# Performance work log

Measured on AMD Instinct MI355X. Metric: run time of the kernel, lower is better.

The kernel has to match this reference:

```python
import jax, jax.numpy as jnp
import numpy as np

# Instant-NGP style multi-level hash encoding constants (match init_kwargs)
N_LEVELS = 16
N_ENC = 16384          # per-level hashmap size (power of two)
N_EMBED = 2
MIN_RES = 16
MAX_RES = 512
HIDDEN = 64
P1 = np.uint32(2654435761)  # spatial hash primes (Instant-NGP)
P2 = np.uint32(805459861)


def _resolutions():
    b = np.exp((np.log(MAX_RES) - np.log(MIN_RES)) / (N_LEVELS - 1))
    return [int(np.floor(MIN_RES * b ** l)) for l in range(N_LEVELS)]


def _hash_encode(x, tables):
    """x: (B,3) in [-1,1]; tables: (L, T, E). Returns (B, L*E)."""
    feats = []
    for l, res in enumerate(_resolutions()):
        xg = (x + 1.0) * (0.5 * (res - 1))          # map [-1,1] -> [0, res-1]
        x0f = jnp.floor(xg)
        w = xg - x0f                                # (B,3) trilinear weights
        i0 = jnp.clip(x0f.astype(jnp.int32), 0, res - 1)
        i1 = jnp.clip(i0 + 1, 0, res - 1)
        dense = (res ** 3) <= N_ENC                 # small levels index densely
        feat = jnp.zeros((x.shape[0], N_EMBED), dtype=x.dtype)
        for cz in (0, 1):
            for cy in (0, 1):
                for cx in (0, 1):
                    ix = i1[:, 0] if cx else i0[:, 0]
                    iy = i1[:, 1] if cy else i0[:, 1]
                    iz = i1[:, 2] if cz else i0[:, 2]
                    if dense:
                        idx = ix + res * (iy + res * iz)
                    else:
                        idx = (ix.astype(jnp.uint32)
                               ^ (iy.astype(jnp.uint32) * P1)
                               ^ (iz.astype(jnp.uint32) * P2)) & np.uint32(N_ENC - 1)
                        idx = idx.astype(jnp.int32)
                    wc = ((w[:, 0] if cx else 1.0 - w[:, 0])
                          * (w[:, 1] if cy else 1.0 - w[:, 1])
                          * (w[:, 2] if cz else 1.0 - w[:, 2]))
                    feat = feat + wc[:, None] * tables[l, idx]
        feats.append(feat)
    return jnp.concatenate(feats, axis=-1)          # (B, 32)


def setup_inputs() -> dict:
    key = jax.random.key(0)
    ks = jax.random.split(key, 10)
    B = 1048576
    x = jax.random.uniform(ks[0], (B, 3), minval=-1.0, maxval=1.0)
    tables = jax.random.uniform(ks[1], (N_LEVELS, N_ENC, N_EMBED),
                                minval=-1e-4, maxval=1e-4)

    def lin(k, fin, fout):
        s = 1.0 / np.sqrt(fin)
        kw, kb = jax.random.split(k)
        return (jax.random.uniform(kw, (fin, fout), minval=-s, maxval=s),
                jax.random.uniform(kb, (fout,), minval=-s, maxval=s))

    w1, b1 = lin(ks[2], N_LEVELS * N_EMBED, HIDDEN)
    w2, b2 = lin(ks[3], HIDDEN, HIDDEN)
    w3, b3 = lin(ks[4], HIDDEN, 16)
    cw1, cb1 = lin(ks[5], 16, HIDDEN)
    cw2, cb2 = lin(ks[6], HIDDEN, HIDDEN)
    cw3, cb3 = lin(ks[7], HIDDEN, HIDDEN)
    cw4, cb4 = lin(ks[8], HIDDEN, 3)
    return {"x": x, "tables": tables,
            "w1": w1, "b1": b1, "w2": w2, "b2": b2, "w3": w3, "b3": b3,
            "cw1": cw1, "cb1": cb1, "cw2": cw2, "cb2": cb2,
            "cw3": cw3, "cb3": cb3, "cw4": cw4, "cb4": cb4}


def reference(x, tables, w1, b1, w2, b2, w3, b3,
              cw1, cb1, cw2, cb2, cw3, cb3, cw4, cb4):
    h = _hash_encode(x, tables)                     # (B, 32)
    d = jax.nn.relu(h @ w1 + b1)
    d = jax.nn.relu(d @ w2 + b2)
    d = d @ w3 + b3                                 # (B, 16)
    c = jax.nn.relu(d @ cw1 + cb1)
    c = jax.nn.relu(c @ cw2 + cb2)
    c = jax.nn.relu(c @ cw3 + cb3)
    c = jax.nn.sigmoid(c @ cw4 + cb4)               # is_hdr=False -> sigmoid
    sigma = jnp.exp(d[:, 0])                        # (B,)
    return sigma, c
```

## Files before the change

kernel.cpp:

```cpp
#include <hip/hip_runtime.h>

typedef __bf16 bf8 __attribute__((ext_vector_type(8)));
typedef float f4 __attribute__((ext_vector_type(4)));
typedef float f32x16 __attribute__((ext_vector_type(16)));
typedef unsigned short us4 __attribute__((ext_vector_type(4)));
typedef unsigned int u32x4 __attribute__((ext_vector_type(4)));

#define MFMA16(a,b,c) __builtin_amdgcn_mfma_f32_16x16x32_bf16((a),(b),(c),0,0,0)
#define MFMA32(a,b,c) __builtin_amdgcn_mfma_f32_32x32x16_bf16((a),(b),(c),0,0,0)

#define BLOCK 512
#define NWAVE 8

__device__ __forceinline__ unsigned short f2bfu(float f){
  __bf16 h = (__bf16)f;
  union { __bf16 b; unsigned short u; } v; v.b = h; return v.u;
}
__device__ __forceinline__ float ubfu(unsigned int u16){
  union { unsigned int i; float f; } v; v.i = u16 << 16; return v.f;
}

__device__ __forceinline__ void wfence(){
  asm volatile("s_waitcnt lgkmcnt(0)" ::: "memory");
}

#define SBAR() __builtin_amdgcn_sched_barrier(0)

#define OFF_W1   0
#define OFF_W2   2048
#define OFF_W3   6144
#define OFF_CW1  7168
#define OFF_CW2  8192
#define OFF_CW3  12288
#define OFF_CW4  16384
#define OFF_ACT  17408
#define ACT_STRIDE 72
#define SMEM_US  (17408 + NWAVE*16*ACT_STRIDE)

#define BO_B1  0
#define BO_B2  64
#define BO_B3  128
#define BO_CB1 144
#define BO_CB2 208
#define BO_CB3 272
#define BO_CB4 336

template<int FIN,int FOUT,int KS,int MT>
__device__ __forceinline__ void stage_w(const float* w, unsigned short* dst){
  const int total = KS*MT*512;
  for (int e = threadIdx.x; e < total; e += BLOCK){
    int chunk = e >> 9;
    int s = chunk / MT, t = chunk % MT;
    int le = e & 511;
    int lane = le >> 3, j = le & 7;
    int q = lane >> 4, m = lane & 15;
    int i = s*32 + q*8 + j;
    int o = t*16 + m;
    dst[e] = (i < FIN && o < FOUT) ? f2bfu(w[i*FOUT + o]) : (unsigned short)0;
  }
}

__device__ __forceinline__ void stage_cw1(const float* w, unsigned short* dst){
  for (int e = threadIdx.x; e < 1024; e += BLOCK){
    int t = e >> 8;
    int le = e & 255;
    int lane = le >> 3, j = e & 7;
    int q = lane >> 4, m = lane & 15;
    dst[e] = f2bfu(w[(q*8+j)*64 + t*16 + m]);
  }
}

__device__ __forceinline__ void layer64(const unsigned short* wlds, const unsigned short* bias,
                                        unsigned short* act, int lane, bool relu){
  const int q = lane >> 4, m = lane & 15;
  bf8 b0 = *(const bf8*)(act + m*ACT_STRIDE + q*8);
  bf8 b1 = *(const bf8*)(act + m*ACT_STRIDE + 32 + q*8);
  f4 acc[4];
#pragma unroll
  for (int t = 0; t < 4; ++t){
    f4 c = {0.f,0.f,0.f,0.f};
    c = MFMA16(*(const bf8*)(wlds + ((0*4+t)*64+lane)*8), b0, c);
    c = MFMA16(*(const bf8*)(wlds + ((1*4+t)*64+lane)*8), b1, c);
    acc[t] = c;
  }
#pragma unroll
  for (int t = 0; t < 4; ++t){
    us4 bb = *(const us4*)(bias + t*16 + q*4);
    us4 pk;
#pragma unroll
    for (int r = 0; r < 4; ++r){
      float v = acc[t][r] + ubfu(bb[r]);
      if (relu) v = fmaxf(v, 0.f);
      pk[r] = f2bfu(v);
    }
    *(us4*)(act + m*ACT_STRIDE + t*16 + q*4) = pk;
  }
}

#define STAGE_ALL_WEIGHTS()                                                  \
  stage_w<32,64,1,4>(w1,  smem+OFF_W1);                                      \
  stage_w<64,64,2,4>(w2,  smem+OFF_W2);                                      \
  stage_w<64,16,2,1>(w3,  smem+OFF_W3);                                      \
  stage_cw1(cw1, smem+OFF_CW1);                                              \
  stage_w<64,64,2,4>(cw2, smem+OFF_CW2);                                     \
  stage_w<64,64,2,4>(cw3, smem+OFF_CW3);                                     \
  stage_w<64, 3,2,1>(cw4, smem+OFF_CW4);                                     \
  {                                                                          \
    int t = threadIdx.x;                                                     \
    if (t < 64){                                                             \
      sbias[BO_B1 +t] = f2bfu(b1[t]);                                        \
      sbias[BO_B2 +t] = f2bfu(b2[t]);                                        \
      sbias[BO_CB1+t] = f2bfu(cb1[t]);                                       \
      sbias[BO_CB2+t] = f2bfu(cb2[t]);                                       \
      sbias[BO_CB3+t] = f2bfu(cb3[t]);                                       \
    }                                                                        \
    if (t < 16) sbias[BO_B3+t] = f2bfu(b3[t]);                               \
    if (t < 3)  sbias[BO_CB4+t] = f2bfu(cb4[t]);                             \
  }

#define MLP_BODY(bfrag, gp)                                                  \
    {                                                                        \
      f4 acc[4];                                                             \
      _Pragma("unroll")                                                      \
      for (int t = 0; t < 4; ++t){                                           \
        f4 c = {0.f,0.f,0.f,0.f};                                            \
        acc[t] = MFMA16(*(const bf8*)(smem + OFF_W1 + (t*64+lane)*8), bfrag, c);\
      }                                                                      \
      _Pragma("unroll")                                                      \
      for (int t = 0; t < 4; ++t){                                           \
        us4 bb = *(const us4*)(sbias + BO_B1 + t*16 + q*4);                  \
        us4 pk;                                                              \
        _Pragma("unroll")                                                    \
        for (int r = 0; r < 4; ++r){                                         \
          float v = fmaxf(acc[t][r] + ubfu(bb[r]), 0.f);                     \
          pk[r] = f2bfu(v);                                                  \
        }                                                                    \
        *(us4*)(act + m*ACT_STRIDE + t*16 + q*4) = pk;                       \
      }                                                                      \
    }                                                                        \
    wfence();                                                                \
    layer64(smem+OFF_W2, sbias+BO_B2, act, lane, true);                      \
    wfence();                                                                \
    {                                                                        \
      bf8 b0 = *(const bf8*)(act + m*ACT_STRIDE + q*8);                      \
      bf8 b1 = *(const bf8*)(act + m*ACT_STRIDE + 32 + q*8);                 \
      f4 c = {0.f,0.f,0.f,0.f};                                              \
      c = MFMA16(*(const bf8*)(smem + OFF_W3 + lane*8), b0, c);              \
      c = MFMA16(*(const bf8*)(smem + OFF_W3 + (64+lane)*8), b1, c);         \
      us4 bb = *(const us4*)(sbias + BO_B3 + q*4);                           \
      us4 pk;                                                                \
      float d0 = 0.f;                                                        \
      _Pragma("unroll")                                                      \
      for (int r = 0; r < 4; ++r){                                           \
        float v = c[r] + ubfu(bb[r]);                                        \
        if (r == 0) d0 = v;                                                  \
        pk[r] = f2bfu(v);                                                    \
      }                                                                      \
      if (q == 0 && gp < nB) out[gp] = expf(d0);                             \
      *(us4*)(act + m*ACT_STRIDE + q*4) = pk;                                \
    }                                                                        \
    wfence();                                                                \
    {                                                                        \
      bf8 bc, aw[4];                                                         \
      if (q < 2){                                                            \
        bc = *(const bf8*)(act + m*ACT_STRIDE + q*8);                        \
        _Pragma("unroll")                                                    \
        for (int t = 0; t < 4; ++t)                                          \
          aw[t] = *(const bf8*)(smem + OFF_CW1 + (t*32+lane)*8);             \
      } else {                                                               \
        _Pragma("unroll")                                                    \
        for (int j = 0; j < 8; ++j) bc[j] = (__bf16)0.f;                     \
        _Pragma("unroll")                                                    \
        for (int t = 0; t < 4; ++t) aw[t] = bc;                              \
      }                                                                      \
      f4 acc[4];                                                             \
      _Pragma("unroll")                                                      \
      for (int t = 0; t < 4; ++t){                                           \
        f4 c = {0.f,0.f,0.f,0.f};                                            \
        acc[t] = MFMA16(aw[t], bc, c);                                       \
      }                                                                      \
      _Pragma("unroll")                                                      \
      for (int t = 0; t < 4; ++t){                                           \
        us4 bb = *(const us4*)(sbias + BO_CB1 + t*16 + q*4);                 \
        us4 pk;                                                              \
        _Pragma("unroll")                                                    \
        for (int r = 0; r < 4; ++r){                                         \
          float v = fmaxf(acc[t][r] + ubfu(bb[r]), 0.f);                     \
          pk[r] = f2bfu(v);                                                  \
        }                                                                    \
        *(us4*)(act + m*ACT_STRIDE + t*16 + q*4) = pk;                       \
      }                                                                      \
    }                                                                        \
    wfence();                                                                \
    layer64(smem+OFF_CW2, sbias+BO_CB2, act, lane, true);                    \
    wfence();                                                                \
    layer64(smem+OFF_CW3, sbias+BO_CB3, act, lane, true);                    \
    wfence();                                                                \
    {                                                                        \
      bf8 b0 = *(const bf8*)(act + m*ACT_STRIDE + q*8);                      \
      bf8 b1 = *(const bf8*)(act + m*ACT_STRIDE + 32 + q*8);                 \
      f4 c = {0.f,0.f,0.f,0.f};                                              \
      c = MFMA16(*(const bf8*)(smem + OFF_CW4 + lane*8), b0, c);             \
      c = MFMA16(*(const bf8*)(smem + OFF_CW4 + (64+lane)*8), b1, c);        \
      if (q == 0 && gp < nB){                                                \
        _Pragma("unroll")                                                    \
        for (int r = 0; r < 3; ++r){                                         \
          float v = c[r] + ubfu(sbias[BO_CB4 + r]);                          \
          out[nB + gp*3 + r] = 1.f/(1.f + expf(-v));                         \
        }                                                                    \
      }                                                                      \
    }                                                                        \
    wfence();

#define CH 16384
__global__ __launch_bounds__(512) void hash_phase(
    const float* __restrict__ xin, const float* __restrict__ tab,
    unsigned int* __restrict__ feat, int nB)
{
  __shared__ unsigned int stab[16384];
  __shared__ int sres[16];
  const int lvl = blockIdx.y;
  {
    const float2* t2 = (const float2*)tab + (lvl<<14);
    for (int e = threadIdx.x; e < 16384; e += 512){
      float2 v = t2[e];
      stab[e] = ((unsigned)f2bfu(v.y) << 16) | (unsigned)f2bfu(v.x);
    }
    if (threadIdx.x < 16){
      const int R[16] = {16,20,25,32,40,50,64,80,101,128,161,203,256,322,406,512};
      sres[threadIdx.x] = R[threadIdx.x];
    }
  }
  __syncthreads();

  const int res = sres[lvl];
  const float sc = 0.5f*(float)(res-1);
  const bool dense = (lvl < 3);
  unsigned int* fout = feat + (size_t)lvl * (size_t)nB;

  int pend = (blockIdx.x + 1) * CH; if (pend > nB) pend = nB;
  for (int p = blockIdx.x*CH + threadIdx.x; p < pend; p += 512){
    const float px = xin[p*3+0], py = xin[p*3+1], pz = xin[p*3+2];
    const float xs=(px+1.f)*sc, ys=(py+1.f)*sc, zs=(pz+1.f)*sc;
    const float fx=floorf(xs), fy=floorf(ys), fz=floorf(zs);
    const float wx=xs-fx, wy=ys-fy, wz=zs-fz;
    int ix0=min(max((int)fx,0),res-1);
    int iy0=min(max((int)fy,0),res-1);
    int iz0=min(max((int)fz,0),res-1);
    int ix1=min(ix0+1,res-1), iy1=min(iy0+1,res-1), iz1=min(iz0+1,res-1);
    unsigned X0,X1,Y0,Y1,Z0,Z1;
    if (dense){
      X0=(unsigned)ix0;            X1=(unsigned)ix1;
      Y0=(unsigned)(res*iy0);      Y1=(unsigned)(res*iy1);
      Z0=(unsigned)(res*res*iz0);  Z1=(unsigned)(res*res*iz1);
    } else {
      X0=(unsigned)ix0;                 X1=(unsigned)ix1;
      Y0=(unsigned)iy0*2654435761u;     Y1=(unsigned)iy1*2654435761u;
      Z0=(unsigned)iz0*805459861u;      Z1=(unsigned)iz1*805459861u;
    }
    const float wx0=1.f-wx, wy0=1.f-wy, wz0=1.f-wz;
    float f0=0.f, f1=0.f;
#pragma unroll
    for (int c = 0; c < 8; ++c){
      unsigned xc = (c&1)?X1:X0;
      unsigned yc = (c&2)?Y1:Y0;
      unsigned zc = (c&4)?Z1:Z0;
      unsigned idx = dense ? (xc+yc+zc) : ((xc^yc^zc)&16383u);
      unsigned tv = stab[idx];
      float wc = ((c&1)?wx:wx0) * ((c&2)?wy:wy0) * ((c&4)?wz:wz0);
      f0 += wc*ubfu(tv << 16);
      f1 += wc*ubfu(tv & 0xffff0000u);
    }
    fout[p] = ((unsigned)f2bfu(f1) << 16) | (unsigned)f2bfu(f0);
  }
}


#define W32_W1   0
#define W32_W2   2048
#define W32_W3   6144
#define W32_CW1  8192
#define W32_CW2  9216
#define W32_CW3  13312
#define W32_CW4  17408
#define W32_TOT  19456

#define SB_B1  0
#define SB_B2  64
#define SB_CB1 128
#define SB_CB2 192
#define SB_CB3 256
#define SB_B3  320
#define SB_CB4 352

template<int FIN,int FOUT,int MT,int KT>
__device__ __forceinline__ void stage32(const float* w, unsigned short* dst){
  const int total = MT*KT*512;
  for (int e = threadIdx.x; e < total; e += BLOCK){
    int frag = e >> 9;
    int mt = frag / KT, kt = frag % KT;
    int l  = (e >> 3) & 63, j = e & 7;
    int i  = kt*16 + ((l >> 5) << 3) + j;
    int o  = mt*32 + (l & 31);
    dst[e] = (i < FIN && o < FOUT) ? f2bfu(w[i*FOUT + o]) : (unsigned short)0;
  }
}

__device__ __forceinline__ unsigned pk2(float x, float y){
  typedef __bf16 bf2v __attribute__((ext_vector_type(2)));
  union { bf2v b; unsigned u; } v;
  v.b[0] = (__bf16)x; v.b[1] = (__bf16)y;
  return v.u;
}

__device__ __forceinline__ bf8 mkbf8(unsigned d0, unsigned d1, unsigned d2, unsigned d3){
  union { u32x4 u; bf8 b; } v;
  v.u[0] = d0; v.u[1] = d1; v.u[2] = d2; v.u[3] = d3;
  return v.b;
}

__device__ __forceinline__ void swap_half(unsigned a, unsigned b, unsigned& x, unsigned& y){
#if __has_builtin(__builtin_amdgcn_permlane32_swap)
  auto r = __builtin_amdgcn_permlane32_swap(a, b, false, false);
  x = r[0]; y = r[1];
#else
  unsigned sa = (unsigned)__shfl_xor((int)a, 32, 64);
  unsigned sb = (unsigned)__shfl_xor((int)b, 32, 64);
  bool lo = (threadIdx.x & 32) == 0;
  x = lo ? a : sb;
  y = lo ? sa : b;
#endif
}

__device__ __forceinline__ f32x16 bias16(const float* sb, int h4){
  f4 c0 = *(const f4*)(sb + h4);
  f4 c1 = *(const f4*)(sb + 8  + h4);
  f4 c2 = *(const f4*)(sb + 16 + h4);
  f4 c3 = *(const f4*)(sb + 24 + h4);
  f32x16 c;
#pragma unroll
  for (int r = 0; r < 4; ++r){
    c[r] = c0[r]; c[4+r] = c1[r]; c[8+r] = c2[r]; c[12+r] = c3[r];
  }
  return c;
}

__device__ __forceinline__ void trans2(const f32x16 a0, const f32x16 a1, bf8* B){
  unsigned p0[8], p1[8];
#pragma unroll
  for (int p = 0; p < 8; ++p){
    p0[p] = pk2(fmaxf(a0[2*p], 0.f), fmaxf(a0[2*p+1], 0.f));
    p1[p] = pk2(fmaxf(a1[2*p], 0.f), fmaxf(a1[2*p+1], 0.f));
  }
#pragma unroll
  for (int o = 0; o < 2; ++o){
    unsigned x0,y0,x1,y1;
    swap_half(p0[4*o+0], p0[4*o+2], x0, y0);
    swap_half(p0[4*o+1], p0[4*o+3], x1, y1);
    B[o] = mkbf8(x0, x1, y0, y1);
    swap_half(p1[4*o+0], p1[4*o+2], x0, y0);
    swap_half(p1[4*o+1], p1[4*o+3], x1, y1);
    B[2+o] = mkbf8(x0, x1, y0, y1);
  }
}

#define PTS_PER_BLOCK 1024
#define M_ITERS 4

__global__ __launch_bounds__(BLOCK, 2) void mlp32_phase(
    const unsigned int* __restrict__ feat,
    const float* __restrict__ w1,  const float* __restrict__ b1,
    const float* __restrict__ w2,  const float* __restrict__ b2,
    const float* __restrict__ w3,  const float* __restrict__ b3,
    const float* __restrict__ cw1, const float* __restrict__ cb1,
    const float* __restrict__ cw2, const float* __restrict__ cb2,
    const float* __restrict__ cw3, const float* __restrict__ cb3,
    const float* __restrict__ cw4, const float* __restrict__ cb4,
    float* __restrict__ out, int nB)
{
  __shared__ __align__(16) unsigned short sw[W32_TOT];
  __shared__ __align__(16) float sbf[384];
  stage32<32,64,2,2>(w1,  sw+W32_W1);
  stage32<64,64,2,4>(w2,  sw+W32_W2);
  stage32<64,16,1,4>(w3,  sw+W32_W3);
  stage32<16,64,2,1>(cw1, sw+W32_CW1);
  stage32<64,64,2,4>(cw2, sw+W32_CW2);
  stage32<64,64,2,4>(cw3, sw+W32_CW3);
  stage32<64, 3,1,4>(cw4, sw+W32_CW4);
  {
    int t = threadIdx.x;
    if (t < 64){
      sbf[SB_B1 +t] = b1[t];
      sbf[SB_B2 +t] = b2[t];
      sbf[SB_CB1+t] = cb1[t];
      sbf[SB_CB2+t] = cb2[t];
      sbf[SB_CB3+t] = cb3[t];
    }
    if (t >= 64 && t < 96)  sbf[SB_B3  + t-64] = (t-64 < 16) ? b3[t-64]  : 0.f;
    if (t >= 96 && t < 128) sbf[SB_CB4 + t-96] = (t-96 < 3)  ? cb4[t-96] : 0.f;
  }
  __syncthreads();

  const int l  = threadIdx.x & 63, wv = threadIdx.x >> 6;
  const int h  = l >> 5, n = l & 31, h4 = h << 2;
  const int base0 = blockIdx.x * PTS_PER_BLOCK + wv*32 + n;

#define FR(off, frag) (*(const bf8*)(sw + (off) + ((frag) << 9) + (l << 3)))
#define LOADF(d0, d1, g) {                                                   \
    int gg = min((g), nB-1);                                                 \
    _Pragma("unroll")                                                        \
    for (int d = 0; d < 4; ++d){                                             \
      d0[d] = feat[(size_t)(h4 + d)*(size_t)nB + gg];                        \
      d1[d] = feat[(size_t)(8 + h4 + d)*(size_t)nB + gg];                    \
    } }

  u32x4 f0, f1, nf0, nf1;
  LOADF(f0, f1, base0)

  for (int it = 0; it < M_ITERS; ++it){
    const int gp = base0 + it*256;
    bf8 B[4];
    B[0] = mkbf8(f0[0], f0[1], f0[2], f0[3]);
    B[1] = mkbf8(f1[0], f1[1], f1[2], f1[3]);
    SBAR();

    f32x16 a0 = bias16(sbf + SB_B1,      h4);
    f32x16 a1 = bias16(sbf + SB_B1 + 32, h4);
    a0 = MFMA32(FR(W32_W1,0), B[0], a0);
    a0 = MFMA32(FR(W32_W1,1), B[1], a0);
    a1 = MFMA32(FR(W32_W1,2), B[0], a1);
    a1 = MFMA32(FR(W32_W1,3), B[1], a1);
    SBAR();

    if (it + 1 < M_ITERS){ LOADF(nf0, nf1, gp + 256) }
    SBAR();

    trans2(a0, a1, B);
    SBAR();

    a0 = bias16(sbf + SB_B2,      h4);
    a1 = bias16(sbf + SB_B2 + 32, h4);
#pragma unroll
    for (int kt = 0; kt < 4; ++kt){
      a0 = MFMA32(FR(W32_W2, kt),   B[kt], a0);
      a1 = MFMA32(FR(W32_W2, 4+kt), B[kt], a1);
    }
    SBAR();
    trans2(a0, a1, B);
    SBAR();

    f32x16 ad = bias16(sbf + SB_B3, h4);
#pragma unroll
    for (int kt = 0; kt < 4; ++kt) ad = MFMA32(FR(W32_W3, kt), B[kt], ad);
    SBAR();
    if (h == 0 && gp < nB) out[gp] = expf(ad[0]);
    {
      unsigned q0 = pk2(ad[0], ad[1]);
      unsigned q1 = pk2(ad[2], ad[3]);
      unsigned q2 = pk2(ad[4], ad[5]);
      unsigned q3 = pk2(ad[6], ad[7]);
      unsigned x0,y0,x1,y1;
      swap_half(q0, q2, x0, y0);
      swap_half(q1, q3, x1, y1);
      B[0] = mkbf8(x0, x1, y0, y1);
    }
    SBAR();

    a0 = bias16(sbf + SB_CB1,      h4);
    a1 = bias16(sbf + SB_CB1 + 32, h4);
    a0 = MFMA32(FR(W32_CW1,0), B[0], a0);
    a1 = MFMA32(FR(W32_CW1,1), B[0], a1);
    SBAR();
    trans2(a0, a1, B);
    SBAR();

    a0 = bias16(sbf + SB_CB2,      h4);
    a1 = bias16(sbf + SB_CB2 + 32, h4);
#pragma unroll
    for (int kt = 0; kt < 4; ++kt){
      a0 = MFMA32(FR(W32_CW2, kt),   B[kt], a0);
      a1 = MFMA32(FR(W32_CW2, 4+kt), B[kt], a1);
    }
    SBAR();
    trans2(a0, a1, B);
    SBAR();

    a0 = bias16(sbf + SB_CB3,      h4);
    a1 = bias16(sbf + SB_CB3 + 32, h4);
#pragma unroll
    for (int kt = 0; kt < 4; ++kt){
      a0 = MFMA32(FR(W32_CW3, kt),   B[kt], a0);
      a1 = MFMA32(FR(W32_CW3, 4+kt), B[kt], a1);
    }
    SBAR();
    trans2(a0, a1, B);
    SBAR();

    f32x16 ac = bias16(sbf + SB_CB4, h4);
#pragma unroll
    for (int kt = 0; kt < 4; ++kt) ac = MFMA32(FR(W32_CW4, kt), B[kt], ac);
    SBAR();
    if (h == 0 && gp < nB){
      out[nB + gp*3 + 0] = 1.f/(1.f + expf(-ac[0]));
      out[nB + gp*3 + 1] = 1.f/(1.f + expf(-ac[1]));
      out[nB + gp*3 + 2] = 1.f/(1.f + expf(-ac[2]));
    }
    SBAR();

    if (it + 1 < M_ITERS){ f0 = nf0; f1 = nf1; }
  }
#undef FR
#undef LOADF
}

__global__ __launch_bounds__(BLOCK) void nerf_fused(
    const float* __restrict__ xin, const float* __restrict__ tab,
    const float* __restrict__ w1,  const float* __restrict__ b1,
    const float* __restrict__ w2,  const float* __restrict__ b2,
    const float* __restrict__ w3,  const float* __restrict__ b3,
    const float* __restrict__ cw1, const float* __restrict__ cb1,
    const float* __restrict__ cw2, const float* __restrict__ cb2,
    const float* __restrict__ cw3, const float* __restrict__ cb3,
    const float* __restrict__ cw4, const float* __restrict__ cb4,
    float* __restrict__ out, int nB)
{
  __shared__ __align__(16) unsigned short smem[SMEM_US];
  __shared__ __align__(16) unsigned short sbias[344];
  __shared__ int sres[16];
  STAGE_ALL_WEIGHTS();
  if (threadIdx.x < 16){
    const int R[16] = {16,20,25,32,40,50,64,80,101,128,161,203,256,322,406,512};
    sres[threadIdx.x] = R[threadIdx.x];
  }
  __syncthreads();

  const int lane = threadIdx.x & 63, wv = threadIdx.x >> 6;
  const int q = lane >> 4, m = lane & 15;
  unsigned short* act = smem + OFF_ACT + wv*16*ACT_STRIDE;

  int res_[4];
#pragma unroll
  for (int d = 0; d < 4; ++d) res_[d] = sres[4*q + d];

  for (int it = 0; it < 4; ++it){
    const int gp  = blockIdx.x*BLOCK + wv*64 + it*16 + m;
    const int gpl = min(gp, nB-1);
    const float px = xin[gpl*3+0];
    const float py = xin[gpl*3+1];
    const float pz = xin[gpl*3+2];

    bf8 bfrag;
#pragma unroll
    for (int d = 0; d < 4; ++d){
      const int lvl = 4*q + d;
      const int res = res_[d];
      const float sc = 0.5f*(float)(res-1);
      const float xs=(px+1.f)*sc, ys=(py+1.f)*sc, zs=(pz+1.f)*sc;
      const float fx=floorf(xs), fy=floorf(ys), fz=floorf(zs);
      const float wx=xs-fx, wy=ys-fy, wz=zs-fz;
      int ix0=min(max((int)fx,0),res-1);
      int iy0=min(max((int)fy,0),res-1);
      int iz0=min(max((int)fz,0),res-1);
      int ix1=min(ix0+1,res-1), iy1=min(iy0+1,res-1), iz1=min(iz0+1,res-1);
      const bool dense = (lvl < 3);
      unsigned X0,X1,Y0,Y1,Z0,Z1;
      if (dense){
        X0=(unsigned)ix0;            X1=(unsigned)ix1;
        Y0=(unsigned)(res*iy0);      Y1=(unsigned)(res*iy1);
        Z0=(unsigned)(res*res*iz0);  Z1=(unsigned)(res*res*iz1);
      } else {
        X0=(unsigned)ix0;                 X1=(unsigned)ix1;
        Y0=(unsigned)iy0*2654435761u;     Y1=(unsigned)iy1*2654435761u;
        Z0=(unsigned)iz0*805459861u;      Z1=(unsigned)iz1*805459861u;
      }
      const float wx0=1.f-wx, wy0=1.f-wy, wz0=1.f-wz;
      float f0=0.f, f1=0.f;
      const float2* tl = (const float2*)tab + (lvl<<14);
#pragma unroll
      for (int c = 0; c < 8; ++c){
        unsigned xc = (c&1)?X1:X0;
        unsigned yc = (c&2)?Y1:Y0;
        unsigned zc = (c&4)?Z1:Z0;
        unsigned idx = dense ? (xc+yc+zc) : ((xc^yc^zc)&16383u);
        float2 tv = tl[idx];
        float wc = ((c&1)?wx:wx0) * ((c&2)?wy:wy0) * ((c&4)?wz:wz0);
        f0 += wc*tv.x;
        f1 += wc*tv.y;
      }
      bfrag[2*d]   = (__bf16)f0;
      bfrag[2*d+1] = (__bf16)f1;
    }
    MLP_BODY(bfrag, gp)
  }
}

extern "C" void kernel_launch(void* const* d_in, const int* in_sizes, int n_in,
                              void* d_out, int out_size, void* d_ws, size_t ws_size,
                              hipStream_t stream) {
  (void)n_in; (void)out_size;
  const int nB = in_sizes[0] / 3;
  const float* xin = (const float*)d_in[0];
  const float* tab = (const float*)d_in[1];
  const float *w1=(const float*)d_in[2],  *b1=(const float*)d_in[3];
  const float *w2=(const float*)d_in[4],  *b2=(const float*)d_in[5];
  const float *w3=(const float*)d_in[6],  *b3=(const float*)d_in[7];
  const float *cw1=(const float*)d_in[8], *cb1=(const float*)d_in[9];
  const float *cw2=(const float*)d_in[10],*cb2=(const float*)d_in[11];
  const float *cw3=(const float*)d_in[12],*cb3=(const float*)d_in[13];
  const float *cw4=(const float*)d_in[14],*cb4=(const float*)d_in[15];
  float* out = (float*)d_out;

  const size_t need = (size_t)nB * 16u * 4u;
  if (ws_size >= need){
    dim3 ga((nB + CH - 1) / CH, 16);
    hash_phase<<<ga, dim3(512), 0, stream>>>(xin, tab, (unsigned int*)d_ws, nB);
    const int blocks = (nB + PTS_PER_BLOCK - 1) / PTS_PER_BLOCK;
    mlp32_phase<<<dim3(blocks), dim3(BLOCK), 0, stream>>>(
        (const unsigned int*)d_ws, w1,b1,w2,b2,w3,b3,
        cw1,cb1,cw2,cb2,cw3,cb3,cw4,cb4, out, nB);
  } else {
    const int blocks = (nB + BLOCK - 1) / BLOCK;
    nerf_fused<<<dim3(blocks), dim3(BLOCK), 0, stream>>>(
        xin, tab, w1,b1,w2,b2,w3,b3,
        cw1,cb1,cw2,cb2,cw3,cb3,cw4,cb4, out, nB);
  }
}
```

Before: 175.3 us.

## Pre-pack hash tables to bf16, unroll hash loop, and keep MLP weights in registers

Adds a tiny pre-pass kernel that converts the hash tables to packed bf16 once, so each hash block loads its level table with 16-byte vector copies instead of converting float2 entries itself. The hash point loop is manually unrolled by two. In the MLP phase, the weight fragments for the small layers are hoisted into registers before the loop, and the 64x64 layer fragments are prefetched into registers ahead of use, which cuts repeated LDS reads. This costs an extra kernel launch and higher register pressure, which may lower occupancy.

New measurement: 179.6 us. 1.02x slower.

```diff
diff --git a/kernel.cpp b/kernel.cpp
--- a/kernel.cpp
+++ b/kernel.cpp
@@ -212,12 +212,85 @@
     }                                                                        \
     wfence();
 
+__global__ __launch_bounds__(512) void tab_pack(
+    const float* __restrict__ tab, unsigned int* __restrict__ tp)
+{
+  int e = blockIdx.x*512 + threadIdx.x;
+  float2 v = ((const float2*)tab)[e];
+  tp[e] = ((unsigned)f2bfu(v.y) << 16) | (unsigned)f2bfu(v.x);
+}
+
 #define CH 16384
+
+#define HASH_BODY_COMMON                                                     \
+  const int res = sres[lvl];                                                 \
+  const float sc = 0.5f*(float)(res-1);                                      \
+  const bool dense = (lvl < 3);                                              \
+  unsigned int* fout = feat + (size_t)lvl * (size_t)nB;                      \
+  auto body = [&](int p){                                                    \
+    const float px = xin[p*3+0], py = xin[p*3+1], pz = xin[p*3+2];           \
+    const float xs=(px+1.f)*sc, ys=(py+1.f)*sc, zs=(pz+1.f)*sc;              \
+    const float fx=floorf(xs), fy=floorf(ys), fz=floorf(zs);                 \
+    const float wx=xs-fx, wy=ys-fy, wz=zs-fz;                                \
+    int ix0=min(max((int)fx,0),res-1);                                       \
+    int iy0=min(max((int)fy,0),res-1);                                       \
+    int iz0=min(max((int)fz,0),res-1);                                       \
+    int ix1=min(ix0+1,res-1), iy1=min(iy0+1,res-1), iz1=min(iz0+1,res-1);    \
+    unsigned X0,X1,Y0,Y1,Z0,Z1;                                              \
+    if (dense){                                                              \
+      X0=(unsigned)ix0;            X1=(unsigned)ix1;                         \
+      Y0=(unsigned)(res*iy0);      Y1=(unsigned)(res*iy1);                   \
+      Z0=(unsigned)(res*res*iz0);  Z1=(unsigned)(res*res*iz1);               \
+    } else {                                                                 \
+      X0=(unsigned)ix0;                 X1=(unsigned)ix1;                    \
+      Y0=(unsigned)iy0*2654435761u;     Y1=(unsigned)iy1*2654435761u;        \
+      Z0=(unsigned)iz0*805459861u;      Z1=(unsigned)iz1*805459861u;         \
+    }                                                                        \
+    const float wx0=1.f-wx, wy0=1.f-wy, wz0=1.f-wz;                          \
+    float f0=0.f, f1=0.f;                                                    \
+    _Pragma("unroll")                                                        \
+    for (int c = 0; c < 8; ++c){                                             \
+      unsigned xc = (c&1)?X1:X0;                                             \
+      unsigned yc = (c&2)?Y1:Y0;                                             \
+      unsigned zc = (c&4)?Z1:Z0;                                             \
+      unsigned idx = dense ? (xc+yc+zc) : ((xc^yc^zc)&16383u);               \
+      unsigned tv = stab[idx];                                               \
+      float wc = ((c&1)?wx:wx0) * ((c&2)?wy:wy0) * ((c&4)?wz:wz0);           \
+      f0 += wc*ubfu(tv << 16);                                               \
+      f1 += wc*ubfu(tv & 0xffff0000u);                                       \
+    }                                                                        \
+    fout[p] = ((unsigned)f2bfu(f1) << 16) | (unsigned)f2bfu(f0);             \
+  };                                                                         \
+  int pend = (blockIdx.x + 1) * CH; if (pend > nB) pend = nB;                \
+  int p = blockIdx.x*CH + threadIdx.x;                                       \
+  for (; p + 512 < pend; p += 1024){ body(p); body(p + 512); }               \
+  if (p < pend) body(p);
+
 __global__ __launch_bounds__(512) void hash_phase(
+    const float* __restrict__ xin, const unsigned int* __restrict__ tabp,
+    unsigned int* __restrict__ feat, int nB)
+{
+  __shared__ __align__(16) unsigned int stab[16384];
+  __shared__ int sres[16];
+  const int lvl = blockIdx.y;
+  {
+    const u32x4* t4 = (const u32x4*)(tabp + (lvl<<14));
+    u32x4* s4 = (u32x4*)stab;
+    for (int e = threadIdx.x; e < 4096; e += 512) s4[e] = t4[e];
+    if (threadIdx.x < 16){
+      const int R[16] = {16,20,25,32,40,50,64,80,101,128,161,203,256,322,406,512};
+      sres[threadIdx.x] = R[threadIdx.x];
+    }
+  }
+  __syncthreads();
+  HASH_BODY_COMMON
+}
+
+__global__ __launch_bounds__(512) void hash_phase_f32(
     const float* __restrict__ xin, const float* __restrict__ tab,
     unsigned int* __restrict__ feat, int nB)
 {
-  __shared__ unsigned int stab[16384];
+  __shared__ __align__(16) unsigned int stab[16384];
   __shared__ int sres[16];
   const int lvl = blockIdx.y;
   {
@@ -232,47 +305,7 @@
     }
   }
   __syncthreads();
-
-  const int res = sres[lvl];
-  const float sc = 0.5f*(float)(res-1);
-  const bool dense = (lvl < 3);
-  unsigned int* fout = feat + (size_t)lvl * (size_t)nB;
-
-  int pend = (blockIdx.x + 1) * CH; if (pend > nB) pend = nB;
-  for (int p = blockIdx.x*CH + threadIdx.x; p < pend; p += 512){
-    const float px = xin[p*3+0], py = xin[p*3+1], pz = xin[p*3+2];
-    const float xs=(px+1.f)*sc, ys=(py+1.f)*sc, zs=(pz+1.f)*sc;
-    const float fx=floorf(xs), fy=floorf(ys), fz=floorf(zs);
-    const float wx=xs-fx, wy=ys-fy, wz=zs-fz;
-    int ix0=min(max((int)fx,0),res-1);
-    int iy0=min(max((int)fy,0),res-1);
-    int iz0=min(max((int)fz,0),res-1);
-    int ix1=min(ix0+1,res-1), iy1=min(iy0+1,res-1), iz1=min(iz0+1,res-1);
-    unsigned X0,X1,Y0,Y1,Z0,Z1;
-    if (dense){
-      X0=(unsigned)ix0;            X1=(unsigned)ix1;
-      Y0=(unsigned)(res*iy0);      Y1=(unsigned)(res*iy1);
-      Z0=(unsigned)(res*res*iz0);  Z1=(unsigned)(res*res*iz1);
-    } else {
-      X0=(unsigned)ix0;                 X1=(unsigned)ix1;
-      Y0=(unsigned)iy0*2654435761u;     Y1=(unsigned)iy1*2654435761u;
-      Z0=(unsigned)iz0*805459861u;      Z1=(unsigned)iz1*805459861u;
-    }
-    const float wx0=1.f-wx, wy0=1.f-wy, wz0=1.f-wz;
-    float f0=0.f, f1=0.f;
-#pragma unroll
-    for (int c = 0; c < 8; ++c){
-      unsigned xc = (c&1)?X1:X0;
-      unsigned yc = (c&2)?Y1:Y0;
-      unsigned zc = (c&4)?Z1:Z0;
-      unsigned idx = dense ? (xc+yc+zc) : ((xc^yc^zc)&16383u);
-      unsigned tv = stab[idx];
-      float wc = ((c&1)?wx:wx0) * ((c&2)?wy:wy0) * ((c&4)?wz:wz0);
-      f0 += wc*ubfu(tv << 16);
-      f1 += wc*ubfu(tv & 0xffff0000u);
-    }
-    fout[p] = ((unsigned)f2bfu(f1) << 16) | (unsigned)f2bfu(f0);
-  }
+  HASH_BODY_COMMON
 }
 
 
@@ -414,6 +447,15 @@
       d1[d] = feat[(size_t)(8 + h4 + d)*(size_t)nB + gg];                    \
     } }
 
+  bf8 w1f[4], w3f[4], cw1f[2], cw4f[4];
+#pragma unroll
+  for (int t = 0; t < 4; ++t) w1f[t]  = FR(W32_W1,  t);
+#pragma unroll
+  for (int t = 0; t < 4; ++t) w3f[t]  = FR(W32_W3,  t);
+  cw1f[0] = FR(W32_CW1, 0); cw1f[1] = FR(W32_CW1, 1);
+#pragma unroll
+  for (int t = 0; t < 4; ++t) cw4f[t] = FR(W32_CW4, t);
+
   u32x4 f0, f1, nf0, nf1;
   LOADF(f0, f1, base0)
 
@@ -424,12 +466,15 @@
     B[1] = mkbf8(f1[0], f1[1], f1[2], f1[3]);
     SBAR();
 
+    bf8 wf[8];
+#pragma unroll
+    for (int k = 0; k < 8; ++k) wf[k] = FR(W32_W2, k);
     f32x16 a0 = bias16(sbf + SB_B1,      h4);
     f32x16 a1 = bias16(sbf + SB_B1 + 32, h4);
-    a0 = MFMA32(FR(W32_W1,0), B[0], a0);
-    a0 = MFMA32(FR(W32_W1,1), B[1], a0);
-    a1 = MFMA32(FR(W32_W1,2), B[0], a1);
-    a1 = MFMA32(FR(W32_W1,3), B[1], a1);
+    a0 = MFMA32(w1f[0], B[0], a0);
+    a0 = MFMA32(w1f[1], B[1], a0);
+    a1 = MFMA32(w1f[2], B[0], a1);
+    a1 = MFMA32(w1f[3], B[1], a1);
     SBAR();
 
     if (it + 1 < M_ITERS){ LOADF(nf0, nf1, gp + 256) }
@@ -442,16 +487,19 @@
     a1 = bias16(sbf + SB_B2 + 32, h4);
 #pragma unroll
     for (int kt = 0; kt < 4; ++kt){
-      a0 = MFMA32(FR(W32_W2, kt),   B[kt], a0);
-      a1 = MFMA32(FR(W32_W2, 4+kt), B[kt], a1);
+      a0 = MFMA32(wf[kt],   B[kt], a0);
+      a1 = MFMA32(wf[4+kt], B[kt], a1);
     }
     SBAR();
     trans2(a0, a1, B);
     SBAR();
 
+    bf8 wg[8];
+#pragma unroll
+    for (int k = 0; k < 8; ++k) wg[k] = FR(W32_CW2, k);
     f32x16 ad = bias16(sbf + SB_B3, h4);
 #pragma unroll
-    for (int kt = 0; kt < 4; ++kt) ad = MFMA32(FR(W32_W3, kt), B[kt], ad);
+    for (int kt = 0; kt < 4; ++kt) ad = MFMA32(w3f[kt], B[kt], ad);
     SBAR();
     if (h == 0 && gp < nB) out[gp] = expf(ad[0]);
     {
@@ -468,18 +516,20 @@
 
     a0 = bias16(sbf + SB_CB1,      h4);
     a1 = bias16(sbf + SB_CB1 + 32, h4);
-    a0 = MFMA32(FR(W32_CW1,0), B[0], a0);
-    a1 = MFMA32(FR(W32_CW1,1), B[0], a1);
+    a0 = MFMA32(cw1f[0], B[0], a0);
+    a1 = MFMA32(cw1f[1], B[0], a1);
     SBAR();
     trans2(a0, a1, B);
     SBAR();
 
+#pragma unroll
+    for (int k = 0; k < 8; ++k) wf[k] = FR(W32_CW3, k);
     a0 = bias16(sbf + SB_CB2,      h4);
     a1 = bias16(sbf + SB_CB2 + 32, h4);
 #pragma unroll
     for (int kt = 0; kt < 4; ++kt){
-      a0 = MFMA32(FR(W32_CW2, kt),   B[kt], a0);
-      a1 = MFMA32(FR(W32_CW2, 4+kt), B[kt], a1);
+      a0 = MFMA32(wg[kt],   B[kt], a0);
+      a1 = MFMA32(wg[4+kt], B[kt], a1);
     }
     SBAR();
     trans2(a0, a1, B);
@@ -489,8 +539,8 @@
     a1 = bias16(sbf + SB_CB3 + 32, h4);
 #pragma unroll
     for (int kt = 0; kt < 4; ++kt){
-      a0 = MFMA32(FR(W32_CW3, kt),   B[kt], a0);
-      a1 = MFMA32(FR(W32_CW3, 4+kt), B[kt], a1);
+      a0 = MFMA32(wf[kt],   B[kt], a0);
+      a1 = MFMA32(wf[4+kt], B[kt], a1);
     }
     SBAR();
     trans2(a0, a1, B);
@@ -498,7 +548,7 @@
 
     f32x16 ac = bias16(sbf + SB_CB4, h4);
 #pragma unroll
-    for (int kt = 0; kt < 4; ++kt) ac = MFMA32(FR(W32_CW4, kt), B[kt], ac);
+    for (int kt = 0; kt < 4; ++kt) ac = MFMA32(cw4f[kt], B[kt], ac);
     SBAR();
     if (h == 0 && gp < nB){
       out[nB + gp*3 + 0] = 1.f/(1.f + expf(-ac[0]));
@@ -610,10 +660,21 @@
   const float *cw4=(const float*)d_in[14],*cb4=(const float*)d_in[15];
   float* out = (float*)d_out;
 
-  const size_t need = (size_t)nB * 16u * 4u;
-  if (ws_size >= need){
+  const size_t need  = (size_t)nB * 16u * 4u;
+  const size_t needp = need + 16u * 16384u * 4u;
+  if (ws_size >= needp){
+    unsigned int* feat = (unsigned int*)d_ws;
+    unsigned int* tabp = feat + (size_t)nB * 16u;
+    tab_pack<<<dim3(512), dim3(512), 0, stream>>>(tab, tabp);
     dim3 ga((nB + CH - 1) / CH, 16);
-    hash_phase<<<ga, dim3(512), 0, stream>>>(xin, tab, (unsigned int*)d_ws, nB);
+    hash_phase<<<ga, dim3(512), 0, stream>>>(xin, tabp, feat, nB);
+    const int blocks = (nB + PTS_PER_BLOCK - 1) / PTS_PER_BLOCK;
+    mlp32_phase<<<dim3(blocks), dim3(BLOCK), 0, stream>>>(
+        feat, w1,b1,w2,b2,w3,b3,
+        cw1,cb1,cw2,cb2,cw3,cb3,cw4,cb4, out, nB);
+  } else if (ws_size >= need){
+    dim3 ga((nB + CH - 1) / CH, 16);
+    hash_phase_f32<<<ga, dim3(512), 0, stream>>>(xin, tab, (unsigned int*)d_ws, nB);
     const int blocks = (nB + PTS_PER_BLOCK - 1) / PTS_PER_BLOCK;
     mlp32_phase<<<dim3(blocks), dim3(BLOCK), 0, stream>>>(
         (const unsigned int*)d_ws, w1,b1,w2,b2,w3,b3,
```
